# Optimization experiments

Hardware: AMD Instinct MI355X
Metric: run time of the kernel (lower is better)

The kernel has to match this reference:

```python
import jax, jax.numpy as jnp
import numpy as np


def _qkernel(r, i, j, k):
    # Build the real-valued block kernel of a quaternion dense layer.
    # r,i,j,k: [in/4, out/4] -> kernel [in, out] implementing the Hamilton product.
    col_r = jnp.concatenate([r, -i, -j, -k], axis=0)
    col_i = jnp.concatenate([i, r, -k, j], axis=0)
    col_j = jnp.concatenate([j, k, r, -i], axis=0)
    col_k = jnp.concatenate([k, -j, i, r], axis=0)
    return jnp.concatenate([col_r, col_i, col_j, col_k], axis=1)


def setup_inputs() -> dict:
    key = jax.random.key(0)
    ks = jax.random.split(key, 12)
    B, F, H = 32768, 1024, 256
    F4, H4 = F // 4, H // 4
    s_in = 1.0 / np.sqrt(F)
    s_h = 1.0 / np.sqrt(H)
    inp = {
        "x": jax.random.normal(ks[0], (B, F), dtype=jnp.float32),
        "wx_r": jax.random.normal(ks[1], (4, F4, H4), dtype=jnp.float32) * s_in,
        "wx_i": jax.random.normal(ks[2], (4, F4, H4), dtype=jnp.float32) * s_in,
        "wx_j": jax.random.normal(ks[3], (4, F4, H4), dtype=jnp.float32) * s_in,
        "wx_k": jax.random.normal(ks[4], (4, F4, H4), dtype=jnp.float32) * s_in,
        "bx": jnp.zeros((4, H), dtype=jnp.float32),
        "uh_r": jax.random.normal(ks[5], (4, H4, H4), dtype=jnp.float32) * s_h,
        "uh_i": jax.random.normal(ks[6], (4, H4, H4), dtype=jnp.float32) * s_h,
        "uh_j": jax.random.normal(ks[7], (4, H4, H4), dtype=jnp.float32) * s_h,
        "uh_k": jax.random.normal(ks[8], (4, H4, H4), dtype=jnp.float32) * s_h,
        "fco_w": jax.random.normal(ks[9], (H, H), dtype=jnp.float32) * s_h,
        "fco_b": jnp.zeros((H,), dtype=jnp.float32),
    }
    return inp


def reference(x, wx_r, wx_i, wx_j, wx_k, bx, uh_r, uh_i, uh_j, uh_k, fco_w, fco_b):
    # Single-step quaternion LSTM cell with zero initial hidden/cell state.
    # Gate order along leading axis: [forget, input, output, cell].
    Kx = jax.vmap(_qkernel)(wx_r, wx_i, wx_j, wx_k)   # [4, F, H]
    Ku = jax.vmap(_qkernel)(uh_r, uh_i, uh_j, uh_k)   # [4, H, H]
    H = bx.shape[1]
    h0 = jnp.zeros((x.shape[0], H), dtype=x.dtype)
    c0 = h0
    gx = jnp.einsum('bf,gfh->gbh', x, Kx) + bx[:, None, :]   # [4, B, H]
    gu = jnp.einsum('bh,ghk->gbk', h0, Ku)                    # [4, B, H]
    z = gx + gu
    ft = jax.nn.sigmoid(z[0])
    it = jax.nn.sigmoid(z[1])
    ot = jax.nn.sigmoid(z[2])
    at = z[3]
    c = it * jnp.tanh(at) + ft * c0
    h = ot * jnp.tanh(c)
    return h @ fco_w + fco_b
```

## Files before the change

### kernel.cpp

```cpp
#include <hip/hip_runtime.h>
#include <cstdint>
#include <cstddef>

#define WS_WP   0
#define WS_FCO  1572864
#define WS_BP   1703936
#define WS_HVP  1707008
#define WS_XP   18484224
#define WS_NEED 85593088ull

typedef __attribute__((ext_vector_type(8))) __bf16 bf16x8;
typedef __attribute__((ext_vector_type(4))) __bf16 bf16x4;
typedef __attribute__((ext_vector_type(4))) float floatx4;

__device__ __forceinline__ unsigned short f2bf(float f) {
  unsigned int u = __builtin_bit_cast(unsigned int, f);
  u += 0x7fffu + ((u >> 16) & 1u);
  return (unsigned short)(u >> 16);
}

__device__ __forceinline__ float sigmf(float z) {
  return __builtin_amdgcn_rcpf(1.f + __expf(-z));
}
__device__ __forceinline__ float tanh_(float z) {
  return 1.f - 2.f * __builtin_amdgcn_rcpf(1.f + __expf(2.f * z));
}

__device__ __forceinline__ void gld16(const void* g, void* l) {
  __builtin_amdgcn_global_load_lds(
      (const __attribute__((address_space(1))) unsigned int*)g,
      (__attribute__((address_space(3))) unsigned int*)l, 16, 0, 0);
}

__global__ __launch_bounds__(256) void pack_k(
    const float* __restrict__ wr, const float* __restrict__ wi,
    const float* __restrict__ wj, const float* __restrict__ wk,
    const float* __restrict__ bx, const float* __restrict__ fw,
    const float* __restrict__ x,
    unsigned short* __restrict__ Wp, unsigned short* __restrict__ Fp,
    float* __restrict__ bp, unsigned short* __restrict__ xp) {
  int t = threadIdx.x;
  if (blockIdx.x < 384) {
    int gpp = blockIdx.x >> 7;
    int oct = blockIdx.x & 127;
    int gp = gpp + 1;
    int h = t;
    int hb = h >> 6, hr = h & 63;
    int f0 = oct << 3;
    int fb = f0 >> 8, fr0 = f0 & 255;
    const int   comp_t[4][4] = {{0,1,2,3},{1,0,3,2},{2,3,0,1},{3,2,1,0}};
    const float sign_t[4][4] = {{1.f,-1.f,-1.f,-1.f},{1.f,1.f,-1.f,1.f},
                                {1.f,1.f,1.f,-1.f},{1.f,-1.f,1.f,1.f}};
    const float* srcs[4] = {wr, wi, wj, wk};
    const float* s = srcs[comp_t[hb][fb]] + ((size_t)((gp << 8) + fr0)) * 64 + hr;
    float sg = sign_t[hb][fb];
    unsigned short v[8];
#pragma unroll
    for (int j = 0; j < 8; ++j) v[j] = f2bf(sg * s[(size_t)j * 64]);
    int c = h * 3 + gpp;
    int cb = c / 192, nl = c % 192;
    int kb = oct >> 2, q = oct & 3;
    int idx16 = (nl << 2) + (q ^ ((nl >> 1) & 3));
    uint4 val = make_uint4(
        (unsigned)v[0] | ((unsigned)v[1] << 16), (unsigned)v[2] | ((unsigned)v[3] << 16),
        (unsigned)v[4] | ((unsigned)v[5] << 16), (unsigned)v[6] | ((unsigned)v[7] << 16));
    *(uint4*)(Wp + (size_t)(cb * 32 + kb) * 6144 + idx16 * 8) = val;
    if (oct == 0) bp[c] = bx[(gp << 8) + h];
  } else if (blockIdx.x < 416) {
    int oct = blockIdx.x - 384;
    int n = t;
    int k0 = oct << 3;
    unsigned short v[8];
#pragma unroll
    for (int j = 0; j < 8; ++j) v[j] = f2bf(fw[(size_t)(k0 + j) * 256 + n]);
    int nb = n >> 7, nl = n & 127, kb = oct >> 2, q = oct & 3;
    int idx16 = (nl << 2) + (q ^ ((nl >> 1) & 3));
    uint4 val = make_uint4(
        (unsigned)v[0] | ((unsigned)v[1] << 16), (unsigned)v[2] | ((unsigned)v[3] << 16),
        (unsigned)v[4] | ((unsigned)v[5] << 16), (unsigned)v[6] | ((unsigned)v[7] << 16));
    *(uint4*)(Fp + (size_t)((nb << 3) + kb) * 4096 + idx16 * 8) = val;
  } else {
    int b = blockIdx.x - 416;
    int mb = b >> 3, kb8 = b & 7;
    const float* xb = x + (size_t)mb * 128 * 1024 + kb8 * 128;
    unsigned short* xpb = xp + ((size_t)mb * 32 + (size_t)kb8 * 4) * 4096;
#pragma unroll
    for (int i = 0; i < 8; ++i) {
      int s = t + i * 256;
      int tile = s >> 9, idx16 = s & 511;
      int ml = idx16 >> 2;
      int q = (idx16 & 3) ^ ((ml >> 1) & 3);
      const float* src = xb + (size_t)ml * 1024 + tile * 32 + q * 8;
      float4 a0 = *(const float4*)src;
      float4 a1 = *(const float4*)(src + 4);
      uint4 val = make_uint4(
          (unsigned)f2bf(a0.x) | ((unsigned)f2bf(a0.y) << 16),
          (unsigned)f2bf(a0.z) | ((unsigned)f2bf(a0.w) << 16),
          (unsigned)f2bf(a1.x) | ((unsigned)f2bf(a1.y) << 16),
          (unsigned)f2bf(a1.z) | ((unsigned)f2bf(a1.w) << 16));
      *(uint4*)(xpb + (size_t)tile * 4096 + idx16 * 8) = val;
    }
  }
}

__global__ __launch_bounds__(256, 2) void gemm1_xp_k(
    const unsigned short* __restrict__ xp, const unsigned short* __restrict__ Wp,
    const float* __restrict__ bp, unsigned short* __restrict__ hvp) {
  __shared__ char smem[61440];
  float* zep = (float*)smem;

  const int t = threadIdx.x;
  const int lane = t & 63, wid = t >> 6;
  const int wm = wid >> 1, wn = wid & 1;
  const int lrow = lane & 15, q = lane >> 4;
  const int rowt = blockIdx.x;
  const int cby = blockIdx.y;
  const unsigned short* apb = xp + (size_t)rowt * 32 * 4096;
  const unsigned short* wpb = Wp + (size_t)cby * 32 * 6144;

  floatx4 acc[4][6];
#pragma unroll
  for (int i = 0; i < 4; ++i)
#pragma unroll
    for (int j = 0; j < 6; ++j) acc[i][j] = (floatx4){0.f, 0.f, 0.f, 0.f};

#define STAGE(bufi, kt)                                                       \
  {                                                                           \
    char* base_ = smem + (bufi) * 20480;                                      \
    unsigned short* sA_ = (unsigned short*)base_;                             \
    unsigned short* sB_ = (unsigned short*)(base_ + 8192);                    \
    const unsigned short* at_ = apb + (size_t)(kt) * 4096;                    \
    const unsigned short* bt_ = wpb + (size_t)(kt) * 6144;                    \
    gld16(at_ + t * 8, sA_ + t * 8);                                          \
    gld16(at_ + (t + 256) * 8, sA_ + (t + 256) * 8);                          \
    _Pragma("unroll")                                                         \
    for (int i_ = 0; i_ < 3; ++i_) {                                          \
      int s_ = t + i_ * 256;                                                  \
      gld16(bt_ + s_ * 8, sB_ + s_ * 8);                                      \
    }                                                                         \
  }
#define COMPUTE(bufi)                                                         \
  {                                                                           \
    const unsigned short* sA_ = (const unsigned short*)(smem + (bufi) * 20480);\
    const unsigned short* sB_ = sA_ + 4096;                                   \
    bf16x8 af[4], bf[6];                                                      \
    _Pragma("unroll")                                                         \
    for (int mt = 0; mt < 4; ++mt) {                                          \
      int m = wm * 64 + mt * 16 + lrow;                                       \
      int slot = (m << 2) + (q ^ ((m >> 1) & 3));                             \
      af[mt] = *(const bf16x8*)(const void*)(sA_ + slot * 8);                 \
    }                                                                         \
    _Pragma("unroll")                                                         \
    for (int nt = 0; nt < 6; ++nt) {                                          \
      int n = wn * 96 + nt * 16 + lrow;                                       \
      int off16 = (n << 2) + (q ^ ((n >> 1) & 3));                            \
      bf[nt] = *(const bf16x8*)(const void*)(sB_ + off16 * 8);                \
    }                                                                         \
    _Pragma("unroll")                                                         \
    for (int mt = 0; mt < 4; ++mt)                                            \
      _Pragma("unroll")                                                       \
      for (int nt = 0; nt < 6; ++nt)                                          \
        acc[mt][nt] = __builtin_amdgcn_mfma_f32_16x16x32_bf16(                \
            af[mt], bf[nt], acc[mt][nt], 0, 0, 0);                            \
  }

  STAGE(0, 0)
  STAGE(1, 1)
  asm volatile("s_waitcnt vmcnt(5)" ::: "memory");
  __builtin_amdgcn_s_barrier();
  asm volatile("" ::: "memory");

  for (int kt = 0; kt < 32; ++kt) {
    if (kt < 30) STAGE((kt + 2) % 3, kt + 2)
    COMPUTE(kt % 3)
    if (kt < 30) {
      asm volatile("s_waitcnt vmcnt(5)" ::: "memory");
    } else {
      asm volatile("s_waitcnt vmcnt(0)" ::: "memory");
    }
    asm volatile("s_waitcnt lgkmcnt(0)" ::: "memory");
    __builtin_amdgcn_s_barrier();
    asm volatile("" ::: "memory");
  }
#undef COMPUTE
#undef STAGE
  __syncthreads();

  const float* bp0 = bp + cby * 192;
  const int er = t >> 3, oc = t & 7;
#pragma unroll
  for (int pass = 0; pass < 4; ++pass) {
    if (wm == (pass >> 1)) {
      int mtb = (pass & 1) * 2;
#pragma unroll
      for (int mi = 0; mi < 2; ++mi)
#pragma unroll
        for (int nt = 0; nt < 6; ++nt)
#pragma unroll
          for (int r = 0; r < 4; ++r)
            zep[(mi * 16 + q * 4 + r) * 201 + wn * 96 + nt * 16 + lrow] = acc[mtb + mi][nt][r];
    }
    __syncthreads();
    {
      int ml = pass * 32 + er;
      unsigned short v[8];
#pragma unroll
      for (int j = 0; j < 8; ++j) {
        int hl = oc * 8 + j;
        float zi = zep[er * 201 + hl * 3 + 0] + bp0[hl * 3 + 0];
        float zo = zep[er * 201 + hl * 3 + 1] + bp0[hl * 3 + 1];
        float zc = zep[er * 201 + hl * 3 + 2] + bp0[hl * 3 + 2];
        float it = sigmf(zi);
        float ot = sigmf(zo);
        float cc = it * tanh_(zc);
        v[j] = f2bf(ot * tanh_(cc));
      }
      int ktile = cby * 2 + (oc >> 2), qq = oc & 3;
      int idx16 = (ml << 2) + (qq ^ ((ml >> 1) & 3));
      uint4 val = make_uint4(
          (unsigned)v[0] | ((unsigned)v[1] << 16), (unsigned)v[2] | ((unsigned)v[3] << 16),
          (unsigned)v[4] | ((unsigned)v[5] << 16), (unsigned)v[6] | ((unsigned)v[7] << 16));
      *(uint4*)(hvp + (size_t)(rowt * 8 + ktile) * 4096 + idx16 * 8) = val;
    }
    __syncthreads();
  }
}

__global__ __launch_bounds__(512, 4) void gemm1_fb_k(
    const float* __restrict__ x, const unsigned short* __restrict__ Wp,
    const float* __restrict__ bp, unsigned short* __restrict__ hvp) {
  __shared__ char smem[57344];
  float* zep = (float*)smem;

  const int t = threadIdx.x;
  const int lane = t & 63, wid = t >> 6;
  const int wm = wid >> 2, wn = wid & 3;
  const int lrow = lane & 15, q = lane >> 4;
  const int rowt = blockIdx.x;
  const int nbq = blockIdx.y;
  const int cb0 = nbq * 2;
  const int row0 = rowt * 64;
  const float* xbase = x + (size_t)row0 * 1024;

  const int sr = t >> 3, kq = t & 7;
  const int sq8 = kq >> 1, shalf = kq & 1;

  floatx4 acc[2][6];
#pragma unroll
  for (int i = 0; i < 2; ++i)
#pragma unroll
    for (int j = 0; j < 6; ++j) acc[i][j] = (floatx4){0.f, 0.f, 0.f, 0.f};

#define STAGE_B(bufi, kt)                                                     \
  {                                                                           \
    unsigned short* sBs_ = (unsigned short*)(smem + (bufi) * 28672 + 4096);   \
    const unsigned short* bt0_ = Wp + ((size_t)cb0 * 32 + (kt)) * 6144;       \
    _Pragma("unroll")                                                         \
    for (int i_ = 0; i_ < 3; ++i_) {                                          \
      int s_ = t + i_ * 512;                                                  \
      int cbL_ = s_ >= 768;                                                   \
      const unsigned short* src_ =                                            \
          bt0_ + (size_t)cbL_ * 196608 + (s_ - cbL_ * 768) * 8;               \
      gld16(src_, sBs_ + s_ * 8);                                             \
    }                                                                         \
  }
#define LOAD_A(ra, kt)                                                        \
  { ra = *(const float4*)(xbase + (size_t)sr * 1024 + (kt) * 32 + kq * 4); }
#define WRITE_A(ra, bufi)                                                     \
  {                                                                           \
    unsigned short* sAs_ = (unsigned short*)(smem + (bufi) * 28672);          \
    int slot_ = (sr << 2) + (sq8 ^ ((sr >> 1) & 3));                          \
    bf16x4 v_;                                                                \
    v_[0] = (__bf16)ra.x; v_[1] = (__bf16)ra.y;                               \
    v_[2] = (__bf16)ra.z; v_[3] = (__bf16)ra.w;                               \
    *(bf16x4*)(sAs_ + slot_ * 8 + shalf * 4) = v_;                            \
  }
#define COMPUTE(bufi)                                                         \
  {                                                                           \
    const unsigned short* sA_ = (const unsigned short*)(smem + (bufi) * 28672);\
    const unsigned short* sB_ = sA_ + 2048;                                   \
    bf16x8 af[2], bf[6];                                                      \
    _Pragma("unroll")                                                         \
    for (int mt = 0; mt < 2; ++mt) {                                          \
      int m = wm * 32 + mt * 16 + lrow;                                       \
      int slot = (m << 2) + (q ^ ((m >> 1) & 3));                             \
      af[mt] = *(const bf16x8*)(const void*)(sA_ + slot * 8);                 \
    }                                                                         \
    _Pragma("unroll")                                                         \
    for (int nt = 0; nt < 6; ++nt) {                                          \
      int nl = (wn & 1) * 96 + nt * 16 + lrow;                                \
      int off16 = (nl << 2) + (q ^ ((nl >> 1) & 3));                          \
      bf[nt] = *(const bf16x8*)(const void*)(                                 \
          sB_ + ((size_t)(wn >> 1) * 768 + off16) * 8);                       \
    }                                                                         \
    _Pragma("unroll")                                                         \
    for (int mt = 0; mt < 2; ++mt)                                            \
      _Pragma("unroll")                                                       \
      for (int nt = 0; nt < 6; ++nt)                                          \
        acc[mt][nt] = __builtin_amdgcn_mfma_f32_16x16x32_bf16(                \
            af[mt], bf[nt], acc[mt][nt], 0, 0, 0);                            \
  }

  float4 ra;
  LOAD_A(ra, 0)
  STAGE_B(0, 0)
  WRITE_A(ra, 0)
  __syncthreads();

  for (int kt = 0; kt < 32; ++kt) {
    if (kt < 31) {
      LOAD_A(ra, kt + 1)
      STAGE_B((kt + 1) & 1, kt + 1)
    }
    COMPUTE(kt & 1)
    if (kt < 31) WRITE_A(ra, (kt + 1) & 1)
    __syncthreads();
  }
#undef COMPUTE
#undef STAGE_B
#undef LOAD_A
#undef WRITE_A

  const float* bp0 = bp + cb0 * 192;
  const int er = t >> 4, oc = t & 15;
  const int cbL = oc >> 3, oo = oc & 7;
  const int mb128 = rowt >> 1;
#pragma unroll
  for (int pass = 0; pass < 2; ++pass) {
    if (wm == pass) {
#pragma unroll
      for (int mt = 0; mt < 2; ++mt)
#pragma unroll
        for (int nt = 0; nt < 6; ++nt)
#pragma unroll
          for (int r = 0; r < 4; ++r)
            zep[(mt * 16 + q * 4 + r) * 385 + wn * 96 + nt * 16 + lrow] = acc[mt][nt][r];
    }
    __syncthreads();
    {
      int ml = (rowt & 1) * 64 + pass * 32 + er;
      unsigned short v[8];
#pragma unroll
      for (int j = 0; j < 8; ++j) {
        int hl = oo * 8 + j;
        int cz = cbL * 192 + hl * 3;
        float zi = zep[er * 385 + cz + 0] + bp0[cz + 0];
        float zo = zep[er * 385 + cz + 1] + bp0[cz + 1];
        float zc = zep[er * 385 + cz + 2] + bp0[cz + 2];
        float it = sigmf(zi);
        float ot = sigmf(zo);
        float cc = it * tanh_(zc);
        v[j] = f2bf(ot * tanh_(cc));
      }
      int ktile = (cb0 + cbL) * 2 + (oo >> 2), qq = oo & 3;
      int idx16 = (ml << 2) + (qq ^ ((ml >> 1) & 3));
      uint4 val = make_uint4(
          (unsigned)v[0] | ((unsigned)v[1] << 16), (unsigned)v[2] | ((unsigned)v[3] << 16),
          (unsigned)v[4] | ((unsigned)v[5] << 16), (unsigned)v[6] | ((unsigned)v[7] << 16));
      *(uint4*)(hvp + (size_t)(mb128 * 8 + ktile) * 4096 + idx16 * 8) = val;
    }
    __syncthreads();
  }
}

__global__ __launch_bounds__(256, 4) void gemm2_k(
    const unsigned short* __restrict__ hvp, const unsigned short* __restrict__ Fp,
    const float* __restrict__ fcob, float* __restrict__ out) {
  __shared__ unsigned short sB[32768];
  const int t = threadIdx.x;
  const int lane = t & 63, wid = t >> 6;
  const int wm = wid >> 1, wn = wid & 1;
  const int lrow = lane & 15, q = lane >> 4;
  const int mb = blockIdx.x, nb = blockIdx.y;

  const unsigned short* fpb = Fp + (size_t)nb * 32768;
#pragma unroll
  for (int i = 0; i < 16; ++i) gld16(fpb + (t + i * 256) * 8, sB + (t + i * 256) * 8);

  floatx4 acc[4][4];
#pragma unroll
  for (int i = 0; i < 4; ++i)
#pragma unroll
    for (int j = 0; j < 4; ++j) acc[i][j] = (floatx4){0.f, 0.f, 0.f, 0.f};
  __syncthreads();

#pragma unroll
  for (int kt = 0; kt < 8; ++kt) {
    const unsigned short* at_ = hvp + (size_t)(mb * 8 + kt) * 4096;
    bf16x8 af[4], bf[4];
#pragma unroll
    for (int mt = 0; mt < 4; ++mt) {
      int m = wm * 64 + mt * 16 + lrow;
      int o = (m << 2) + (q ^ ((m >> 1) & 3));
      af[mt] = *(const bf16x8*)(const void*)(at_ + o * 8);
    }
#pragma unroll
    for (int nt = 0; nt < 4; ++nt) {
      int n = wn * 64 + nt * 16 + lrow;
      int o = (n << 2) + (q ^ ((n >> 1) & 3));
      bf[nt] = *(const bf16x8*)(const void*)(sB + kt * 4096 + o * 8);
    }
#pragma unroll
    for (int mt = 0; mt < 4; ++mt)
#pragma unroll
      for (int nt = 0; nt < 4; ++nt)
        acc[mt][nt] = __builtin_amdgcn_mfma_f32_16x16x32_bf16(af[mt], bf[nt], acc[mt][nt], 0, 0, 0);
  }
#pragma unroll
  for (int nt = 0; nt < 4; ++nt) {
    int colg = nb * 128 + wn * 64 + nt * 16 + lrow;
    float bias = fcob[colg];
#pragma unroll
    for (int mt = 0; mt < 4; ++mt) {
      int rowg = mb * 128 + wm * 64 + mt * 16 + q * 4;
#pragma unroll
      for (int r = 0; r < 4; ++r)
        out[(size_t)(rowg + r) * 256 + colg] = acc[mt][nt][r] + bias;
    }
  }
}

extern "C" void kernel_launch(void* const* d_in, const int* in_sizes, int n_in,
                              void* d_out, int out_size, void* d_ws, size_t ws_size,
                              hipStream_t stream) {
  const float* x  = (const float*)d_in[0];
  const float* wr = (const float*)d_in[1];
  const float* wi = (const float*)d_in[2];
  const float* wj = (const float*)d_in[3];
  const float* wk = (const float*)d_in[4];
  const float* bx = (const float*)d_in[5];
  const float* fw = (const float*)d_in[10];
  const float* fb = (const float*)d_in[11];
  char* ws = (char*)d_ws;
  unsigned short* Wp  = (unsigned short*)(ws + WS_WP);
  unsigned short* Fp  = (unsigned short*)(ws + WS_FCO);
  float*          bp  = (float*)(ws + WS_BP);
  unsigned short* hvp = (unsigned short*)(ws + WS_HVP);
  float*          out = (float*)d_out;

  const bool big = ws_size >= WS_NEED;
  unsigned short* xp = big ? (unsigned short*)(ws + WS_XP) : hvp;

  hipLaunchKernelGGL(pack_k, dim3(big ? 2464 : 416), dim3(256), 0, stream,
                     wr, wi, wj, wk, bx, fw, x, Wp, Fp, bp, xp);
  if (big) {
    hipLaunchKernelGGL(gemm1_xp_k, dim3(256, 4), dim3(256), 0, stream, xp, Wp, bp, hvp);
  } else {
    hipLaunchKernelGGL(gemm1_fb_k, dim3(512, 2), dim3(512), 0, stream, x, Wp, bp, hvp);
  }
  hipLaunchKernelGGL(gemm2_k, dim3(256, 2), dim3(256), 0, stream, hvp, Fp, fb, out);
}
```

Measured before the change: 298.9 us.

## Double waves per block in xp GEMM and halve each wave's N tile

The first GEMM kernel now runs 512 threads (8 waves in a 2x4 grid) instead of 256. Each wave computes a 64x48 output tile instead of 64x96, which halves its accumulators and B fragments. The global-to-LDS staging loads and vmcnt waits are redistributed across the extra waves, and the epilogue now runs in two passes of 64 rows. The aim is more waves for latency hiding, but launch_bounds(512,4) caps per-wave registers tightly, which risks spills, and the 60 KB of LDS per block still limits how many blocks fit on a CU.

```diff
diff --git a/kernel.cpp b/kernel.cpp
--- a/kernel.cpp
+++ b/kernel.cpp
@@ -103,7 +103,7 @@
   }
 }
 
-__global__ __launch_bounds__(256, 2) void gemm1_xp_k(
+__global__ __launch_bounds__(512, 4) void gemm1_xp_k(
     const unsigned short* __restrict__ xp, const unsigned short* __restrict__ Wp,
     const float* __restrict__ bp, unsigned short* __restrict__ hvp) {
   __shared__ char smem[61440];
@@ -111,18 +111,18 @@
 
   const int t = threadIdx.x;
   const int lane = t & 63, wid = t >> 6;
-  const int wm = wid >> 1, wn = wid & 1;
+  const int wm = wid >> 2, wn = wid & 3;
   const int lrow = lane & 15, q = lane >> 4;
   const int rowt = blockIdx.x;
   const int cby = blockIdx.y;
   const unsigned short* apb = xp + (size_t)rowt * 32 * 4096;
   const unsigned short* wpb = Wp + (size_t)cby * 32 * 6144;
 
-  floatx4 acc[4][6];
+  floatx4 acc[4][3];
 #pragma unroll
   for (int i = 0; i < 4; ++i)
 #pragma unroll
-    for (int j = 0; j < 6; ++j) acc[i][j] = (floatx4){0.f, 0.f, 0.f, 0.f};
+    for (int j = 0; j < 3; ++j) acc[i][j] = (floatx4){0.f, 0.f, 0.f, 0.f};
 
 #define STAGE(bufi, kt)                                                       \
   {                                                                           \
@@ -132,18 +132,23 @@
     const unsigned short* at_ = apb + (size_t)(kt) * 4096;                    \
     const unsigned short* bt_ = wpb + (size_t)(kt) * 6144;                    \
     gld16(at_ + t * 8, sA_ + t * 8);                                          \
-    gld16(at_ + (t + 256) * 8, sA_ + (t + 256) * 8);                          \
-    _Pragma("unroll")                                                         \
-    for (int i_ = 0; i_ < 3; ++i_) {                                          \
-      int s_ = t + i_ * 256;                                                  \
-      gld16(bt_ + s_ * 8, sB_ + s_ * 8);                                      \
+    gld16(bt_ + t * 8, sB_ + t * 8);                                          \
+    if (wid < 4) gld16(bt_ + (t + 512) * 8, sB_ + (t + 512) * 8);             \
+  }
+#define WAITK(kt)                                                             \
+  {                                                                           \
+    if ((kt) < 30) {                                                          \
+      if (wid < 4) { asm volatile("s_waitcnt vmcnt(3)" ::: "memory"); }       \
+      else         { asm volatile("s_waitcnt vmcnt(2)" ::: "memory"); }       \
+    } else {                                                                  \
+      asm volatile("s_waitcnt vmcnt(0)" ::: "memory");                        \
     }                                                                         \
   }
 #define COMPUTE(bufi)                                                         \
   {                                                                           \
     const unsigned short* sA_ = (const unsigned short*)(smem + (bufi) * 20480);\
     const unsigned short* sB_ = sA_ + 4096;                                   \
-    bf16x8 af[4], bf[6];                                                      \
+    bf16x8 af[4], bf[3];                                                      \
     _Pragma("unroll")                                                         \
     for (int mt = 0; mt < 4; ++mt) {                                          \
       int m = wm * 64 + mt * 16 + lrow;                                       \
@@ -151,58 +156,55 @@
       af[mt] = *(const bf16x8*)(const void*)(sA_ + slot * 8);                 \
     }                                                                         \
     _Pragma("unroll")                                                         \
-    for (int nt = 0; nt < 6; ++nt) {                                          \
-      int n = wn * 96 + nt * 16 + lrow;                                       \
+    for (int nt = 0; nt < 3; ++nt) {                                          \
+      int n = wn * 48 + nt * 16 + lrow;                                       \
       int off16 = (n << 2) + (q ^ ((n >> 1) & 3));                            \
       bf[nt] = *(const bf16x8*)(const void*)(sB_ + off16 * 8);                \
     }                                                                         \
     _Pragma("unroll")                                                         \
     for (int mt = 0; mt < 4; ++mt)                                            \
       _Pragma("unroll")                                                       \
-      for (int nt = 0; nt < 6; ++nt)                                          \
+      for (int nt = 0; nt < 3; ++nt)                                          \
         acc[mt][nt] = __builtin_amdgcn_mfma_f32_16x16x32_bf16(                \
             af[mt], bf[nt], acc[mt][nt], 0, 0, 0);                            \
   }
 
   STAGE(0, 0)
   STAGE(1, 1)
-  asm volatile("s_waitcnt vmcnt(5)" ::: "memory");
+  if (wid < 4) { asm volatile("s_waitcnt vmcnt(3)" ::: "memory"); }
+  else         { asm volatile("s_waitcnt vmcnt(2)" ::: "memory"); }
   __builtin_amdgcn_s_barrier();
   asm volatile("" ::: "memory");
 
   for (int kt = 0; kt < 32; ++kt) {
     if (kt < 30) STAGE((kt + 2) % 3, kt + 2)
     COMPUTE(kt % 3)
-    if (kt < 30) {
-      asm volatile("s_waitcnt vmcnt(5)" ::: "memory");
-    } else {
-      asm volatile("s_waitcnt vmcnt(0)" ::: "memory");
-    }
+    WAITK(kt)
     asm volatile("s_waitcnt lgkmcnt(0)" ::: "memory");
     __builtin_amdgcn_s_barrier();
     asm volatile("" ::: "memory");
   }
 #undef COMPUTE
+#undef WAITK
 #undef STAGE
   __syncthreads();
 
   const float* bp0 = bp + cby * 192;
   const int er = t >> 3, oc = t & 7;
 #pragma unroll
-  for (int pass = 0; pass < 4; ++pass) {
-    if (wm == (pass >> 1)) {
-      int mtb = (pass & 1) * 2;
-#pragma unroll
-      for (int mi = 0; mi < 2; ++mi)
-#pragma unroll
-        for (int nt = 0; nt < 6; ++nt)
+  for (int pass = 0; pass < 2; ++pass) {
+    if (wm == pass) {
+#pragma unroll
+      for (int mt = 0; mt < 4; ++mt)
+#pragma unroll
+        for (int nt = 0; nt < 3; ++nt)
 #pragma unroll
           for (int r = 0; r < 4; ++r)
-            zep[(mi * 16 + q * 4 + r) * 201 + wn * 96 + nt * 16 + lrow] = acc[mtb + mi][nt][r];
+            zep[(mt * 16 + q * 4 + r) * 201 + wn * 48 + nt * 16 + lrow] = acc[mt][nt][r];
     }
     __syncthreads();
     {
-      int ml = pass * 32 + er;
+      int ml = pass * 64 + er;
       unsigned short v[8];
 #pragma unroll
       for (int j = 0; j < 8; ++j) {
@@ -444,7 +446,7 @@
   hipLaunchKernelGGL(pack_k, dim3(big ? 2464 : 416), dim3(256), 0, stream,
                      wr, wi, wj, wk, bx, fw, x, Wp, Fp, bp, xp);
   if (big) {
-    hipLaunchKernelGGL(gemm1_xp_k, dim3(256, 4), dim3(256), 0, stream, xp, Wp, bp, hvp);
+    hipLaunchKernelGGL(gemm1_xp_k, dim3(256, 4), dim3(512), 0, stream, xp, Wp, bp, hvp);
   } else {
     hipLaunchKernelGGL(gemm1_fb_k, dim3(512, 2), dim3(512), 0, stream, x, Wp, bp, hvp);
   }
```

After: 299.4 us. Within noise of the previous version (+0.2%).

## Interleave LDS fragment loads with MFMA in main GEMM loop and prefetch A in FC GEMM

Applied to the files above, without the earlier changes.

The main gate GEMM loop now splits each k-tile into two halves. It loads A plus half of the B fragments, issues the next global stage, runs half of the MFMAs under raised wave priority, then loads the remaining B fragments before the second half. Explicit s_barrier and sched_barrier calls keep waves in lockstep so LDS reads overlap with MFMA work. The final FC GEMM now software-prefetches the next k-tile's A fragments from global memory into registers, hiding global load latency. The trade-off is more barriers per iteration and higher register pressure.

```diff
diff --git a/kernel.cpp b/kernel.cpp
--- a/kernel.cpp
+++ b/kernel.cpp
@@ -139,30 +139,6 @@
       gld16(bt_ + s_ * 8, sB_ + s_ * 8);                                      \
     }                                                                         \
   }
-#define COMPUTE(bufi)                                                         \
-  {                                                                           \
-    const unsigned short* sA_ = (const unsigned short*)(smem + (bufi) * 20480);\
-    const unsigned short* sB_ = sA_ + 4096;                                   \
-    bf16x8 af[4], bf[6];                                                      \
-    _Pragma("unroll")                                                         \
-    for (int mt = 0; mt < 4; ++mt) {                                          \
-      int m = wm * 64 + mt * 16 + lrow;                                       \
-      int slot = (m << 2) + (q ^ ((m >> 1) & 3));                             \
-      af[mt] = *(const bf16x8*)(const void*)(sA_ + slot * 8);                 \
-    }                                                                         \
-    _Pragma("unroll")                                                         \
-    for (int nt = 0; nt < 6; ++nt) {                                          \
-      int n = wn * 96 + nt * 16 + lrow;                                       \
-      int off16 = (n << 2) + (q ^ ((n >> 1) & 3));                            \
-      bf[nt] = *(const bf16x8*)(const void*)(sB_ + off16 * 8);                \
-    }                                                                         \
-    _Pragma("unroll")                                                         \
-    for (int mt = 0; mt < 4; ++mt)                                            \
-      _Pragma("unroll")                                                       \
-      for (int nt = 0; nt < 6; ++nt)                                          \
-        acc[mt][nt] = __builtin_amdgcn_mfma_f32_16x16x32_bf16(                \
-            af[mt], bf[nt], acc[mt][nt], 0, 0, 0);                            \
-  }
 
   STAGE(0, 0)
   STAGE(1, 1)
@@ -171,18 +147,60 @@
   asm volatile("" ::: "memory");
 
   for (int kt = 0; kt < 32; ++kt) {
+    const unsigned short* sA_ = (const unsigned short*)(smem + (kt % 3) * 20480);
+    const unsigned short* sB_ = sA_ + 4096;
+    bf16x8 af[4], bf[6];
+#pragma unroll
+    for (int mt = 0; mt < 4; ++mt) {
+      int m = wm * 64 + mt * 16 + lrow;
+      int slot = (m << 2) + (q ^ ((m >> 1) & 3));
+      af[mt] = *(const bf16x8*)(const void*)(sA_ + slot * 8);
+    }
+#pragma unroll
+    for (int nt = 0; nt < 3; ++nt) {
+      int n = wn * 96 + nt * 16 + lrow;
+      int off16 = (n << 2) + (q ^ ((n >> 1) & 3));
+      bf[nt] = *(const bf16x8*)(const void*)(sB_ + off16 * 8);
+    }
     if (kt < 30) STAGE((kt + 2) % 3, kt + 2)
-    COMPUTE(kt % 3)
+    __builtin_amdgcn_s_barrier();
+    asm volatile("s_waitcnt lgkmcnt(0)" ::: "memory");
+    __builtin_amdgcn_sched_barrier(0);
+    __builtin_amdgcn_s_setprio(1);
+#pragma unroll
+    for (int mt = 0; mt < 4; ++mt)
+#pragma unroll
+      for (int nt = 0; nt < 3; ++nt)
+        acc[mt][nt] = __builtin_amdgcn_mfma_f32_16x16x32_bf16(
+            af[mt], bf[nt], acc[mt][nt], 0, 0, 0);
+    __builtin_amdgcn_s_setprio(0);
+    __builtin_amdgcn_sched_barrier(0);
+    __builtin_amdgcn_s_barrier();
+#pragma unroll
+    for (int nt = 3; nt < 6; ++nt) {
+      int n = wn * 96 + nt * 16 + lrow;
+      int off16 = (n << 2) + (q ^ ((n >> 1) & 3));
+      bf[nt] = *(const bf16x8*)(const void*)(sB_ + off16 * 8);
+    }
     if (kt < 30) {
       asm volatile("s_waitcnt vmcnt(5)" ::: "memory");
     } else {
       asm volatile("s_waitcnt vmcnt(0)" ::: "memory");
     }
+    __builtin_amdgcn_s_barrier();
     asm volatile("s_waitcnt lgkmcnt(0)" ::: "memory");
+    __builtin_amdgcn_sched_barrier(0);
+    __builtin_amdgcn_s_setprio(1);
+#pragma unroll
+    for (int mt = 0; mt < 4; ++mt)
+#pragma unroll
+      for (int nt = 3; nt < 6; ++nt)
+        acc[mt][nt] = __builtin_amdgcn_mfma_f32_16x16x32_bf16(
+            af[mt], bf[nt], acc[mt][nt], 0, 0, 0);
+    __builtin_amdgcn_s_setprio(0);
+    __builtin_amdgcn_sched_barrier(0);
     __builtin_amdgcn_s_barrier();
-    asm volatile("" ::: "memory");
-  }
-#undef COMPUTE
+  }
 #undef STAGE
   __syncthreads();
 
@@ -382,18 +400,32 @@
   for (int i = 0; i < 4; ++i)
 #pragma unroll
     for (int j = 0; j < 4; ++j) acc[i][j] = (floatx4){0.f, 0.f, 0.f, 0.f};
+
+  int aoff[4];
+#pragma unroll
+  for (int mt = 0; mt < 4; ++mt) {
+    int m = wm * 64 + mt * 16 + lrow;
+    aoff[mt] = ((m << 2) + (q ^ ((m >> 1) & 3))) * 8;
+  }
+  bf16x8 afc[4];
+  {
+    const unsigned short* at_ = hvp + (size_t)(mb * 8) * 4096;
+#pragma unroll
+    for (int mt = 0; mt < 4; ++mt)
+      afc[mt] = *(const bf16x8*)(const void*)(at_ + aoff[mt]);
+  }
   __syncthreads();
 
 #pragma unroll
   for (int kt = 0; kt < 8; ++kt) {
-    const unsigned short* at_ = hvp + (size_t)(mb * 8 + kt) * 4096;
-    bf16x8 af[4], bf[4];
-#pragma unroll
-    for (int mt = 0; mt < 4; ++mt) {
-      int m = wm * 64 + mt * 16 + lrow;
-      int o = (m << 2) + (q ^ ((m >> 1) & 3));
-      af[mt] = *(const bf16x8*)(const void*)(at_ + o * 8);
-    }
+    bf16x8 afn[4];
+    if (kt < 7) {
+      const unsigned short* at_ = hvp + (size_t)(mb * 8 + kt + 1) * 4096;
+#pragma unroll
+      for (int mt = 0; mt < 4; ++mt)
+        afn[mt] = *(const bf16x8*)(const void*)(at_ + aoff[mt]);
+    }
+    bf16x8 bf[4];
 #pragma unroll
     for (int nt = 0; nt < 4; ++nt) {
       int n = wn * 64 + nt * 16 + lrow;
@@ -404,7 +436,11 @@
     for (int mt = 0; mt < 4; ++mt)
 #pragma unroll
       for (int nt = 0; nt < 4; ++nt)
-        acc[mt][nt] = __builtin_amdgcn_mfma_f32_16x16x32_bf16(af[mt], bf[nt], acc[mt][nt], 0, 0, 0);
+        acc[mt][nt] = __builtin_amdgcn_mfma_f32_16x16x32_bf16(afc[mt], bf[nt], acc[mt][nt], 0, 0, 0);
+    if (kt < 7) {
+#pragma unroll
+      for (int mt = 0; mt < 4; ++mt) afc[mt] = afn[mt];
+    }
   }
 #pragma unroll
   for (int nt = 0; nt < 4; ++nt) {
```

New measurement: 301.1 us. Within noise of the previous version (+0.7%).
